# Performance work log

Hardware: AMD Instinct MI355X
Metric: run time of the kernel (lower is better)

Reference implementation:

```python
import jax, jax.numpy as jnp
import numpy as np

B, C = 16384, 2048
DELTA_REL = 0.1


def setup_inputs() -> dict:
    key = jax.random.key(0)
    k1, k2, k3 = jax.random.split(key, 3)
    logits = jax.random.normal(k1, (B, C), dtype=jnp.float32)
    u = jax.random.uniform(k2, (B, C), dtype=jnp.float32)
    lab = (jax.random.uniform(k3, (B, C)) > 0.7).astype(jnp.float32)
    targets = jnp.where(u < 0.4, jnp.float32(jnp.nan), lab)
    return {"logits": logits, "targets": targets, "epoch": 3}


def _large_loss_rejection(logits, targets, epoch):
    unknown = jnp.isnan(targets)
    # unknown_to_negative: NaN -> 0 (negative label)
    t = jnp.where(unknown, 0.0, targets)
    # stable BCE-with-logits: softplus(x) - x*t
    losses = jax.nn.softplus(logits) - logits * t

    # --- no-grad mask construction ---
    ul = jax.lax.stop_gradient(losses) * unknown.astype(losses.dtype)
    percent = jnp.minimum(epoch * DELTA_REL, 1.0).astype(jnp.float32)
    n_unknown = jnp.count_nonzero(ul)
    k = jnp.round(n_unknown.astype(jnp.float32) * percent).astype(jnp.int32)
    k = jnp.maximum(k, 1)
    # k-th largest value of flattened unknown losses = topk(k).values.min()
    sorted_desc = jnp.sort(ul.reshape(-1))[::-1]
    loss_threshold = jax.lax.dynamic_slice(sorted_desc, (k - 1,), (1,))[0]
    lambdas = jnp.where(ul > loss_threshold, 0.0, 1.0)

    return losses * lambdas  # reduction='none'


def reference(logits, targets, epoch):
    return _large_loss_rejection(logits, targets, epoch)
```

## Files before the change

### kernel.cpp

```cpp
#include <hip/hip_runtime.h>
#include <math.h>

typedef float    f32x4 __attribute__((ext_vector_type(4)));
typedef unsigned u32x4 __attribute__((ext_vector_type(4)));

#define HC_OFF     0u
#define H12_OFF    16384u
#define H64_OFF    20480u
#define CTRL_OFF   20544u
#define ZERO_WORDS 20560u
#define CAND_OFF   20560u
#define CAND_CAP   900000u
#define LBUF       2048u

#define FLOOR_BITS 0x36000000u

__device__ __forceinline__ float softplus_exact(float x) {
    float ax = fabsf(x);
    float e = (float)exp(-(double)ax);
    float l = (float)log1p((double)e);
    return fmaxf(x, 0.0f) + l;
}
__device__ __forceinline__ unsigned exact_bits(float x) {
    return __float_as_uint(softplus_exact(x));
}

__device__ __forceinline__ unsigned refine_core(float x, float ax, float e,
                                                float sp) {
    unsigned cb = __float_as_uint(sp);
    float mf = 64.0f + 8.0f * ax;
    if (x < 0.0f) mf += __builtin_amdgcn_rcpf(e);
    bool need = (cb < FLOOR_BITS) || (mf >= 524288.0f);
    if (!need) {
        unsigned m = (unsigned)mf;
        unsigned low = cb & 0xFFFFFu;
        need = (low < m) || (low >= 0x100000u - m);
    }
    if (need) cb = exact_bits(x);
    return cb;
}
__device__ __forceinline__ unsigned refine_A(float x, float* spo) {
    float ax = fabsf(x);
    float e = __expf(-ax);
    float sp = fmaxf(x, 0.0f) + __logf(1.0f + e);
    *spo = sp;
    return refine_core(x, ax, e, sp);
}

__device__ __forceinline__ unsigned kA_elem(float x, float t,
                                            unsigned* __restrict__ sh) {
    float ax = fabsf(x);
    float e = __expf(-ax);
    float sp = fmaxf(x, 0.0f) + __logf(1.0f + e);
    unsigned outb;
    if (isnan(t)) {
        unsigned cb = refine_core(x, ax, e, sp);
        if (cb != 0u) atomicAdd(&sh[cb >> 20], 1u);
        outb = cb;
    } else {
        float loss = sp - x * t;
        outb = __float_as_uint(loss) ^ 0x80000000u;
    }
    return outb;
}

__global__ __launch_bounds__(256) void kA_store_hist(
    const float* __restrict__ lg, const float* __restrict__ tg,
    float* __restrict__ out, unsigned* __restrict__ ws, long long n) {
    __shared__ unsigned sh[4096];
    for (int i = threadIdx.x; i < 4096; i += 256) sh[i] = 0;
    __syncthreads();

    long long n8 = n >> 3;
    long long tid = (long long)blockIdx.x * 256 + threadIdx.x;
    long long stride = (long long)gridDim.x * 256;
    const f32x4* lg4 = (const f32x4*)lg;
    const f32x4* tg4 = (const f32x4*)tg;
    f32x4* out4 = (f32x4*)out;

    long long i = tid;
    f32x4 xa, xb, ta, tb;
    if (i < n8) {
        xa = lg4[2 * i];
        xb = lg4[2 * i + 1];
        ta = __builtin_nontemporal_load(&tg4[2 * i]);
        tb = __builtin_nontemporal_load(&tg4[2 * i + 1]);
    }
    while (i < n8) {
        long long j = i + stride;
        f32x4 nxa, nxb, nta, ntb;
        if (j < n8) {
            nxa = lg4[2 * j];
            nxb = lg4[2 * j + 1];
            nta = __builtin_nontemporal_load(&tg4[2 * j]);
            ntb = __builtin_nontemporal_load(&tg4[2 * j + 1]);
        }
        f32x4 oa, ob_;
        oa.x = __uint_as_float(kA_elem(xa.x, ta.x, sh));
        oa.y = __uint_as_float(kA_elem(xa.y, ta.y, sh));
        oa.z = __uint_as_float(kA_elem(xa.z, ta.z, sh));
        oa.w = __uint_as_float(kA_elem(xa.w, ta.w, sh));
        ob_.x = __uint_as_float(kA_elem(xb.x, tb.x, sh));
        ob_.y = __uint_as_float(kA_elem(xb.y, tb.y, sh));
        ob_.z = __uint_as_float(kA_elem(xb.z, tb.z, sh));
        ob_.w = __uint_as_float(kA_elem(xb.w, tb.w, sh));
        out4[2 * i] = oa;
        out4[2 * i + 1] = ob_;
        xa = nxa; xb = nxb; ta = nta; tb = ntb;
        i = j;
    }
    if (tid == 0) {
        for (long long q = (n8 << 3); q < n; ++q)
            out[q] = __uint_as_float(kA_elem(lg[q], tg[q], sh));
    }
    __syncthreads();
    unsigned* hist12 = ws + H12_OFF;
    for (int q = threadIdx.x; q < 4096; q += 256)
        if (sh[q]) atomicAdd(&hist12[q], sh[q]);
}

__global__ __launch_bounds__(256) void k2_sel12(
    unsigned* __restrict__ ws, const int* __restrict__ epoch_ptr) {
    const unsigned* hist12 = ws + H12_OFF;
    unsigned* ctrl = ws + CTRL_OFF;
    __shared__ unsigned long long chunk[256];
    int t = threadIdx.x;
    unsigned long long s = 0;
    for (int j = 0; j < 16; ++j) s += hist12[t * 16 + j];
    chunk[t] = s;
    __syncthreads();
    if (t == 0) {
        unsigned long long tot = 0;
        for (int c = 0; c < 256; ++c) tot += chunk[c];
        int epoch = epoch_ptr[0];
        float percent = fminf((float)epoch * 0.1f, 1.0f);
        float nf = (float)tot;
        float kr = rintf(nf * percent);
        long long k = (long long)kr;
        if (k < 1) k = 1;

        long long cum = 0;
        int b = -1;
        long long kprime = 0;
        for (int c = 255; c >= 0; --c) {
            if (cum + (long long)chunk[c] >= k) {
                long long cc = cum;
                for (int j = 15; j >= 0; --j) {
                    unsigned v = hist12[c * 16 + j];
                    if (cc + (long long)v >= k) {
                        b = c * 16 + j;
                        kprime = k - cc;
                        break;
                    }
                    cc += v;
                }
                break;
            }
            cum += chunk[c];
        }
        ctrl[0] = (unsigned)b;
        ctrl[1] = (unsigned)kprime;
        if (b < 0) {
            ctrl[2] = 0u;
            ctrl[4] = 0xFFFFFFFFu;
            ctrl[6] = 0u;
        } else {
            unsigned lo12 = (unsigned)b << 20;
            double vlo = (double)__uint_as_float(lo12);
            double vhi = (double)__uint_as_float(lo12 + 0xFFFFFu);
            double mb = 1e9;
            if (vlo > 1e-30) {
                double xlo = vlo + log1p(-exp(-vlo)) - 0.001;
                double xhi = vhi + log1p(-exp(-vhi)) + 0.001;
                double axmax = fmax(fabs(xlo), fabs(xhi));
                mb = 64.0 + 8.0 * ceil(axmax);
                if (xlo < 0.0) mb += exp(fmin(-xlo, 30.0));
                mb *= 2.0;
            }
            ctrl[6] = (mb >= 8192.0) ? 8192u : (unsigned)mb;
        }
    }
}

__global__ __launch_bounds__(256) void kB_hist64(
    const float* __restrict__ lg, const unsigned* __restrict__ ob,
    unsigned* __restrict__ ws, long long n) {
    unsigned b12 = ws[CTRL_OFF + 0];
    if (b12 == 0xFFFFFFFFu) return;
    unsigned lo12 = b12 << 20;
    unsigned hi12 = lo12 + (1u << 20);
    unsigned m = ws[CTRL_OFF + 6];

    __shared__ unsigned sh[64];
    __shared__ float buf[LBUF];
    __shared__ unsigned lcnt, gbase;
    if (threadIdx.x < 64) sh[threadIdx.x] = 0;
    if (threadIdx.x == 0) lcnt = 0;
    __syncthreads();

    float* cand = (float*)(ws + CAND_OFF);
    unsigned* cnt = ws + CTRL_OFF + 3;

    long long n4 = n >> 2;
    long long tid = (long long)blockIdx.x * 256 + threadIdx.x;
    long long stride = (long long)gridDim.x * 256;
    const u32x4* o4 = (const u32x4*)ob;

    long long i = tid;
    u32x4 u4;
    if (i < n4) u4 = o4[i];
    while (i < n4) {
        long long j = i + stride;
        u32x4 nu4;
        if (j < n4) nu4 = o4[j];
        unsigned us[4] = {u4.x, u4.y, u4.z, u4.w};
#pragma unroll
        for (int c = 0; c < 4; ++c) {
            unsigned u = us[c];
            if (u != 0u && u >= lo12 && u < hi12) {
                float x = lg[i * 4 + c];
                unsigned rB = u;
                unsigned d = u & 16383u;
                if (d < m || d >= 16384u - m)
                    rB = exact_bits(x);
                atomicAdd(&sh[(rB >> 14) & 63u], 1u);
                unsigned li = atomicAdd(&lcnt, 1u);
                if (li < LBUF) buf[li] = x;
            }
        }
        u4 = nu4;
        i = j;
    }
    if (tid == 0) {
        for (long long q = (n4 << 2); q < n; ++q) {
            unsigned u = ob[q];
            if (u != 0u && u >= lo12 && u < hi12) {
                float x = lg[q];
                unsigned rB = u;
                unsigned d = u & 16383u;
                if (d < m || d >= 16384u - m) rB = exact_bits(x);
                atomicAdd(&sh[(rB >> 14) & 63u], 1u);
                unsigned idx = atomicAdd(cnt, 1u);
                if (idx < CAND_CAP) cand[idx] = x;
            }
        }
    }
    __syncthreads();
    if (threadIdx.x < 64 && sh[threadIdx.x])
        atomicAdd(&ws[H64_OFF + threadIdx.x], sh[threadIdx.x]);
    if (threadIdx.x == 0) {
        unsigned add = (lcnt > LBUF) ? (CAND_CAP + 1u) : lcnt;
        gbase = atomicAdd(cnt, add);
    }
    __syncthreads();
    unsigned c2 = lcnt < LBUF ? lcnt : LBUF;
    for (unsigned q = threadIdx.x; q < c2; q += 256) {
        unsigned gi = gbase + q;
        if (gi < CAND_CAP) cand[gi] = buf[q];
    }
}

__global__ void k4_sel64(unsigned* __restrict__ ws) {
    unsigned* ctrl = ws + CTRL_OFF;
    if (ctrl[0] == 0xFFFFFFFFu) return;
    if (threadIdx.x == 0) {
        long long kprime = (long long)ctrl[1];
        long long cum = 0;
        int s = 0;
        long long kpp = 1;
        for (int j = 63; j >= 0; --j) {
            unsigned v = ws[H64_OFF + j];
            if (cum + (long long)v >= kprime) {
                s = j;
                kpp = kprime - cum;
                break;
            }
            cum += v;
        }
        ctrl[4] = (ctrl[0] << 20) + ((unsigned)s << 14);
        ctrl[5] = (unsigned)kpp;
    }
}

__global__ __launch_bounds__(256) void kC_histwin(
    const float* __restrict__ lg, const unsigned* __restrict__ ob,
    unsigned* __restrict__ ws, long long n) {
    unsigned wlo = ws[CTRL_OFF + 4];
    if (wlo == 0xFFFFFFFFu) return;
    unsigned whi = wlo + 16384u;
    unsigned m = ws[CTRL_OFF + 6];
    unsigned b12 = ws[CTRL_OFF + 0];
    unsigned lo12 = b12 << 20;
    unsigned hi12 = lo12 + (1u << 20);
    unsigned glo = (wlo - lo12 > m) ? wlo - m : lo12;
    unsigned ghi = (hi12 - whi > m) ? whi + m : hi12;
    unsigned count = ws[CTRL_OFF + 3];

    long long tid = (long long)blockIdx.x * 256 + threadIdx.x;
    long long stride = (long long)gridDim.x * 256;

    if (count <= CAND_CAP) {
        const float* cand = (const float*)(ws + CAND_OFF);
        for (long long i = tid; i < (long long)count; i += stride) {
            float x = cand[i];
            float spd;
            unsigned u = refine_A(x, &spd);
            if (u >= glo && u < ghi) {
                unsigned eb = exact_bits(x);
                unsigned rB = u;
                unsigned d = u & 16383u;
                if (d < m || d >= 16384u - m) rB = eb;
                if (rB >= wlo && rB < whi) {
                    unsigned off = eb - wlo;
                    if (off < 16384u) atomicAdd(&ws[HC_OFF + off], 1u);
                }
            }
        }
    } else {
        long long n4 = n >> 2;
        const u32x4* o4 = (const u32x4*)ob;
        for (long long i = tid; i < n4; i += stride) {
            u32x4 u4 = o4[i];
            unsigned us[4] = {u4.x, u4.y, u4.z, u4.w};
#pragma unroll
            for (int c = 0; c < 4; ++c) {
                unsigned u = us[c];
                if (u != 0u && u >= glo && u < ghi) {
                    float x = lg[i * 4 + c];
                    unsigned eb = exact_bits(x);
                    unsigned rB = u;
                    unsigned d = u & 16383u;
                    if (d < m || d >= 16384u - m) rB = eb;
                    if (rB >= wlo && rB < whi) {
                        unsigned off = eb - wlo;
                        if (off < 16384u) atomicAdd(&ws[HC_OFF + off], 1u);
                    }
                }
            }
        }
        if (tid == 0) {
            for (long long i = (n4 << 2); i < n; ++i) {
                unsigned u = ob[i];
                if (u != 0u && u >= glo && u < ghi) {
                    unsigned eb = exact_bits(lg[i]);
                    unsigned rB = u;
                    unsigned d = u & 16383u;
                    if (d < m || d >= 16384u - m) rB = eb;
                    if (rB >= wlo && rB < whi) {
                        unsigned off = eb - wlo;
                        if (off < 16384u) atomicAdd(&ws[HC_OFF + off], 1u);
                    }
                }
            }
        }
    }
}

__global__ __launch_bounds__(1024) void k6_selwin(unsigned* __restrict__ ws) {
    unsigned* ctrl = ws + CTRL_OFF;
    if (ctrl[4] == 0xFFFFFFFFu) return;
    __shared__ unsigned long long csum[1024];
    int t = threadIdx.x;
    unsigned long long s = 0;
    for (int j = 0; j < 16; ++j) s += ws[HC_OFF + t * 16 + j];
    csum[t] = s;
    __syncthreads();
    if (t == 0) {
        long long kpp = (long long)ctrl[5];
        long long cum = 0;
        int sel = 0;
        long long rem = kpp;
        for (int c = 1023; c >= 0; --c) {
            if (cum + (long long)csum[c] >= kpp) {
                sel = c;
                rem = kpp - cum;
                break;
            }
            cum += csum[c];
        }
        long long cc = 0;
        int bsel = 0;
        for (int j = 15; j >= 0; --j) {
            unsigned v = ws[HC_OFF + sel * 16 + j];
            if (cc + (long long)v >= rem) {
                bsel = j;
                break;
            }
            cc += v;
        }
        ctrl[2] = ctrl[4] + (unsigned)(sel * 16 + bsel);
    }
}

__device__ __forceinline__ unsigned kD_elem(unsigned u, unsigned thr,
                                            unsigned m,
                                            const float* __restrict__ lg,
                                            long long idx) {
    if (u & 0x80000000u) return u ^ 0x80000000u;
    unsigned udiff = (u > thr) ? u - thr : thr - u;
    if (udiff <= m) {
        unsigned eb = exact_bits(lg[idx]);
        return (eb > thr) ? 0u : eb;
    }
    return (u > thr) ? 0u : u;
}

__global__ __launch_bounds__(256) void kD_final(
    const float* __restrict__ lg, unsigned* __restrict__ ob,
    const unsigned* __restrict__ ws, long long n) {
    unsigned thr = ws[CTRL_OFF + 2];
    unsigned m = ws[CTRL_OFF + 6];

    long long n8 = n >> 3;
    long long tid = (long long)blockIdx.x * 256 + threadIdx.x;
    long long stride = (long long)gridDim.x * 256;
    u32x4* o4 = (u32x4*)ob;

    long long i = tid;
    u32x4 ua, ub;
    if (i < n8) {
        ua = o4[2 * i];
        ub = o4[2 * i + 1];
    }
    while (i < n8) {
        long long j = i + stride;
        u32x4 nua, nub;
        if (j < n8) {
            nua = o4[2 * j];
            nub = o4[2 * j + 1];
        }
        u32x4 va, vb;
        long long base = i * 8;
        va.x = kD_elem(ua.x, thr, m, lg, base + 0);
        va.y = kD_elem(ua.y, thr, m, lg, base + 1);
        va.z = kD_elem(ua.z, thr, m, lg, base + 2);
        va.w = kD_elem(ua.w, thr, m, lg, base + 3);
        vb.x = kD_elem(ub.x, thr, m, lg, base + 4);
        vb.y = kD_elem(ub.y, thr, m, lg, base + 5);
        vb.z = kD_elem(ub.z, thr, m, lg, base + 6);
        vb.w = kD_elem(ub.w, thr, m, lg, base + 7);
        __builtin_nontemporal_store(va, &o4[2 * i]);
        __builtin_nontemporal_store(vb, &o4[2 * i + 1]);
        ua = nua; ub = nub;
        i = j;
    }
    if (tid == 0) {
        for (long long q = (n8 << 3); q < n; ++q)
            ob[q] = kD_elem(ob[q], thr, m, lg, q);
    }
}

extern "C" void kernel_launch(void* const* d_in, const int* in_sizes, int n_in,
                              void* d_out, int out_size, void* d_ws, size_t ws_size,
                              hipStream_t stream) {
    const float* lg = (const float*)d_in[0];
    const float* tg = (const float*)d_in[1];
    const int* epoch = (const int*)d_in[2];
    float* out = (float*)d_out;
    unsigned* ob = (unsigned*)d_out;
    unsigned* ws = (unsigned*)d_ws;
    long long n = (long long)in_sizes[0];

    (void)hipMemsetAsync(d_ws, 0, (size_t)ZERO_WORDS * 4, stream);

    const int blocks = 2048, threads = 256;
    kA_store_hist<<<blocks, threads, 0, stream>>>(lg, tg, out, ws, n);
    k2_sel12<<<1, 256, 0, stream>>>(ws, epoch);
    kB_hist64<<<blocks, threads, 0, stream>>>(lg, ob, ws, n);
    k4_sel64<<<1, 64, 0, stream>>>(ws);
    kC_histwin<<<1024, threads, 0, stream>>>(lg, ob, ws, n);
    k6_selwin<<<1, 1024, 0, stream>>>(ws);
    kD_final<<<blocks, threads, 0, stream>>>(lg, ob, ws, n);
}
```

Measured before the change: 242.0 us.

## Estimate threshold window from sampled histogram to avoid extra full passes

Adds a sampling pre-pass (one 8-element unit per 512 elements) that builds a coarse and then a sub-bin histogram of unknown losses to estimate a narrow value window around the k-th largest. The main pass then zeroes elements above the window, counts them, and records the indices of in-window elements into a compact gray list. A small exact-selection stage over that list finds the threshold and fixes up those entries. This replaces the later full passes over the output and logits. If the window estimate fails, a fallback path recomputes from the inputs. It adds several small launches and shared-memory atomics in the main pass in exchange for skipping the heavy full-array passes.

```diff
diff --git a/kernel.cpp b/kernel.cpp
--- a/kernel.cpp
+++ b/kernel.cpp
@@ -4,16 +4,25 @@
 typedef float    f32x4 __attribute__((ext_vector_type(4)));
 typedef unsigned u32x4 __attribute__((ext_vector_type(4)));
 
-#define HC_OFF     0u
+#define HBIG_OFF   0u
 #define H12_OFF    16384u
 #define H64_OFF    20480u
-#define CTRL_OFF   20544u
-#define ZERO_WORDS 20560u
-#define CAND_OFF   20560u
-#define CAND_CAP   900000u
+#define SH12_OFF   20544u
+#define SHSUB_OFF  24640u
+#define CTRL_OFF   24840u
+#define FINE_OFF   24864u
+#define ZERO_WORDS 25376u
+#define GRAY_OFF   25376u
+#define GRAY_CAP   440000u
+#define EB_OFF     (GRAY_OFF + GRAY_CAP)
+#define CAND_OFF   25376u
+#define CAND_CAP   880000u
 #define LBUF       2048u
+#define DELTA_S    2500LL
+#define VMARGIN    16384u
 
 #define FLOOR_BITS 0x36000000u
+
 
 __device__ __forceinline__ float softplus_exact(float x) {
     float ax = fabsf(x);
@@ -39,37 +48,202 @@
     if (need) cb = exact_bits(x);
     return cb;
 }
-__device__ __forceinline__ unsigned refine_A(float x, float* spo) {
+__device__ __forceinline__ unsigned refine_A(float x) {
     float ax = fabsf(x);
     float e = __expf(-ax);
     float sp = fmaxf(x, 0.0f) + __logf(1.0f + e);
-    *spo = sp;
     return refine_core(x, ax, e, sp);
 }
-
-__device__ __forceinline__ unsigned kA_elem(float x, float t,
-                                            unsigned* __restrict__ sh) {
+__device__ __forceinline__ unsigned known_loss_bits(float x, float t) {
     float ax = fabsf(x);
     float e = __expf(-ax);
     float sp = fmaxf(x, 0.0f) + __logf(1.0f + e);
-    unsigned outb;
+    return __float_as_uint(sp - x * t);
+}
+
+__global__ __launch_bounds__(256) void k0a_shist(
+    const float* __restrict__ lg, const float* __restrict__ tg,
+    unsigned* __restrict__ ws, long long n) {
+    __shared__ unsigned sh[4096];
+    for (int i = threadIdx.x; i < 4096; i += 256) sh[i] = 0;
+    __syncthreads();
+    long long units = n >> 9;
+    long long u = (long long)blockIdx.x * 256 + threadIdx.x;
+    if (u < units) {
+        const f32x4* lg4 = (const f32x4*)lg;
+        const f32x4* tg4 = (const f32x4*)tg;
+        long long b = u * 128;
+        f32x4 xa = lg4[b], xb = lg4[b + 1];
+        f32x4 ta = tg4[b], tb = tg4[b + 1];
+        float xs[8] = {xa.x, xa.y, xa.z, xa.w, xb.x, xb.y, xb.z, xb.w};
+        float ts[8] = {ta.x, ta.y, ta.z, ta.w, tb.x, tb.y, tb.z, tb.w};
+#pragma unroll
+        for (int c = 0; c < 8; ++c)
+            if (isnan(ts[c])) {
+                unsigned cb = refine_A(xs[c]);
+                if (cb) atomicAdd(&sh[cb >> 20], 1u);
+            }
+    }
+    __syncthreads();
+    for (int i = threadIdx.x; i < 4096; i += 256)
+        if (sh[i]) atomicAdd(&ws[SH12_OFF + i], sh[i]);
+}
+
+__global__ __launch_bounds__(256) void k0b_sbin(
+    unsigned* __restrict__ ws, const int* __restrict__ epoch_ptr) {
+    const unsigned* sh12 = ws + SH12_OFF;
+    unsigned* ctrl = ws + CTRL_OFF;
+    __shared__ unsigned long long chunk[256];
+    int t = threadIdx.x;
+    unsigned long long s = 0;
+    for (int j = 0; j < 16; ++j) s += sh12[t * 16 + j];
+    chunk[t] = s;
+    __syncthreads();
+    if (t == 0) {
+        unsigned long long tot = 0;
+        for (int c = 0; c < 256; ++c) tot += chunk[c];
+        if (tot == 0) {
+            ctrl[7] = 1u;
+            ctrl[8] = 0u; ctrl[9] = 0u; ctrl[19] = 0u;
+            ctrl[17] = 0u; ctrl[18] = 0u;
+            return;
+        }
+        int epoch = epoch_ptr[0];
+        float percent = fminf((float)epoch * 0.1f, 1.0f);
+        long long ks = (long long)((double)percent * (double)tot + 0.5);
+        if (ks < 1) ks = 1;
+        if (ks > (long long)tot) ks = (long long)tot;
+        long long cum = 0;
+        int bE = 0;
+        for (int c = 255; c >= 0; --c) {
+            if (cum + (long long)chunk[c] >= ks) {
+                long long cc = cum;
+                for (int j = 15; j >= 0; --j) {
+                    unsigned v = sh12[c * 16 + j];
+                    if (cc + (long long)v >= ks) { bE = c * 16 + j; break; }
+                    cc += v;
+                }
+                break;
+            }
+            cum += chunk[c];
+        }
+        ctrl[13] = (unsigned)bE;
+        ctrl[17] = (bE > 0) ? (unsigned)(bE - 1) : 0u;
+        ctrl[18] = (bE < 4095) ? (unsigned)(bE + 1) : 4095u;
+        ctrl[19] = (unsigned)ks;
+    }
+}
+
+__global__ __launch_bounds__(256) void k0c_ssub(
+    const float* __restrict__ lg, const float* __restrict__ tg,
+    unsigned* __restrict__ ws, long long n) {
+    if (ws[CTRL_OFF + 7] != 0u) return;
+    unsigned lob = ws[CTRL_OFF + 17], hib = ws[CTRL_OFF + 18];
+    unsigned rlo = lob << 20, rhi = (hib + 1u) << 20;
+    __shared__ unsigned sh[192];
+    if (threadIdx.x < 192) sh[threadIdx.x] = 0;
+    __syncthreads();
+    long long units = n >> 9;
+    long long u = (long long)blockIdx.x * 256 + threadIdx.x;
+    if (u < units) {
+        const f32x4* lg4 = (const f32x4*)lg;
+        const f32x4* tg4 = (const f32x4*)tg;
+        long long b = u * 128;
+        f32x4 xa = lg4[b], xb = lg4[b + 1];
+        f32x4 ta = tg4[b], tb = tg4[b + 1];
+        float xs[8] = {xa.x, xa.y, xa.z, xa.w, xb.x, xb.y, xb.z, xb.w};
+        float ts[8] = {ta.x, ta.y, ta.z, ta.w, tb.x, tb.y, tb.z, tb.w};
+#pragma unroll
+        for (int c = 0; c < 8; ++c)
+            if (isnan(ts[c])) {
+                unsigned cb = refine_A(xs[c]);
+                if (cb >= rlo && cb < rhi && (hib < 4095u || cb >= rlo))
+                    atomicAdd(&sh[(cb - rlo) >> 14], 1u);
+            }
+    }
+    __syncthreads();
+    if (threadIdx.x < 192 && sh[threadIdx.x])
+        atomicAdd(&ws[SHSUB_OFF + threadIdx.x], sh[threadIdx.x]);
+}
+
+__global__ __launch_bounds__(256) void k0d_window(unsigned* __restrict__ ws) {
+    unsigned* ctrl = ws + CTRL_OFF;
+    if (ctrl[7] != 0u) return;
+    __shared__ unsigned long long red[256];
+    __shared__ unsigned arr[192];
+    int t = threadIdx.x;
+    unsigned hib = ctrl[18];
+    unsigned long long s = 0;
+    for (int b = t; b < 4096; b += 256)
+        if ((unsigned)b > hib) s += ws[SH12_OFF + b];
+    red[t] = s;
+    if (t < 192) arr[t] = ws[SHSUB_OFF + t];
+    __syncthreads();
+    for (int off = 128; off > 0; off >>= 1) {
+        if (t < off) red[t] += red[t + off];
+        __syncthreads();
+    }
+    if (t == 0) {
+        unsigned lob = ctrl[17];
+        unsigned base = lob << 20;
+        int nsub = (int)(hib - lob + 1u) * 64;
+        long long ks = (long long)ctrl[19];
+        long long lo_t = ks - DELTA_S;
+        long long hi_t = ks + DELTA_S;
+        long long cum = (long long)red[0];
+        unsigned est_hi = base + ((unsigned)nsub << 14);
+        unsigned est_lo = base;
+        bool fh = false, fl = false;
+        for (int j = nsub - 1; j >= 0; --j) {
+            if (!fh && cum + (long long)arr[j] > lo_t) {
+                est_hi = base + ((unsigned)(j + 1) << 14);
+                fh = true;
+            }
+            cum += arr[j];
+            if (!fl && cum >= hi_t) {
+                est_lo = base + ((unsigned)j << 14);
+                fl = true;
+            }
+            if (fh && fl) break;
+        }
+        if (!fh) est_hi = base;
+        ctrl[8] = est_lo;
+        ctrl[9] = est_hi;
+    }
+}
+
+__device__ __forceinline__ unsigned kA_elem(float x, float t, unsigned idx,
+                                            unsigned* __restrict__ shh,
+                                            unsigned* __restrict__ sha,
+                                            unsigned* __restrict__ buf,
+                                            unsigned* __restrict__ lcnt,
+                                            unsigned elo, unsigned ehi) {
+    float ax = fabsf(x);
+    float e = __expf(-ax);
+    float sp = fmaxf(x, 0.0f) + __logf(1.0f + e);
     if (isnan(t)) {
         unsigned cb = refine_core(x, ax, e, sp);
-        if (cb != 0u) atomicAdd(&sh[cb >> 20], 1u);
-        outb = cb;
-    } else {
-        float loss = sp - x * t;
-        outb = __float_as_uint(loss) ^ 0x80000000u;
-    }
-    return outb;
-}
-
-__global__ __launch_bounds__(256) void kA_store_hist(
+        if (cb != 0u) atomicAdd(&shh[cb >> 20], 1u);
+        if (cb >= ehi) { atomicAdd(sha, 1u); return 0u; }
+        if (cb >= elo) {
+            unsigned li = atomicAdd(lcnt, 1u);
+            if (li < LBUF) buf[li] = idx;
+        }
+        return cb;
+    }
+    return __float_as_uint(sp - x * t);
+}
+
+__global__ __launch_bounds__(256) void kA_main(
     const float* __restrict__ lg, const float* __restrict__ tg,
     float* __restrict__ out, unsigned* __restrict__ ws, long long n) {
-    __shared__ unsigned sh[4096];
-    for (int i = threadIdx.x; i < 4096; i += 256) sh[i] = 0;
-    __syncthreads();
+    __shared__ unsigned shh[4096];
+    __shared__ unsigned buf[LBUF];
+    __shared__ unsigned lcnt, sha, gbase;
+    for (int i = threadIdx.x; i < 4096; i += 256) shh[i] = 0;
+    if (threadIdx.x == 0) { lcnt = 0; sha = 0; }
+    __syncthreads();
+    unsigned elo = ws[CTRL_OFF + 8], ehi = ws[CTRL_OFF + 9];
 
     long long n8 = n >> 3;
     long long tid = (long long)blockIdx.x * 256 + threadIdx.x;
@@ -81,8 +255,7 @@
     long long i = tid;
     f32x4 xa, xb, ta, tb;
     if (i < n8) {
-        xa = lg4[2 * i];
-        xb = lg4[2 * i + 1];
+        xa = lg4[2 * i]; xb = lg4[2 * i + 1];
         ta = __builtin_nontemporal_load(&tg4[2 * i]);
         tb = __builtin_nontemporal_load(&tg4[2 * i + 1]);
     }
@@ -90,36 +263,47 @@
         long long j = i + stride;
         f32x4 nxa, nxb, nta, ntb;
         if (j < n8) {
-            nxa = lg4[2 * j];
-            nxb = lg4[2 * j + 1];
+            nxa = lg4[2 * j]; nxb = lg4[2 * j + 1];
             nta = __builtin_nontemporal_load(&tg4[2 * j]);
             ntb = __builtin_nontemporal_load(&tg4[2 * j + 1]);
         }
+        unsigned base = (unsigned)(i * 8);
         f32x4 oa, ob_;
-        oa.x = __uint_as_float(kA_elem(xa.x, ta.x, sh));
-        oa.y = __uint_as_float(kA_elem(xa.y, ta.y, sh));
-        oa.z = __uint_as_float(kA_elem(xa.z, ta.z, sh));
-        oa.w = __uint_as_float(kA_elem(xa.w, ta.w, sh));
-        ob_.x = __uint_as_float(kA_elem(xb.x, tb.x, sh));
-        ob_.y = __uint_as_float(kA_elem(xb.y, tb.y, sh));
-        ob_.z = __uint_as_float(kA_elem(xb.z, tb.z, sh));
-        ob_.w = __uint_as_float(kA_elem(xb.w, tb.w, sh));
+        oa.x = __uint_as_float(kA_elem(xa.x, ta.x, base + 0, shh, &sha, buf, &lcnt, elo, ehi));
+        oa.y = __uint_as_float(kA_elem(xa.y, ta.y, base + 1, shh, &sha, buf, &lcnt, elo, ehi));
+        oa.z = __uint_as_float(kA_elem(xa.z, ta.z, base + 2, shh, &sha, buf, &lcnt, elo, ehi));
+        oa.w = __uint_as_float(kA_elem(xa.w, ta.w, base + 3, shh, &sha, buf, &lcnt, elo, ehi));
+        ob_.x = __uint_as_float(kA_elem(xb.x, tb.x, base + 4, shh, &sha, buf, &lcnt, elo, ehi));
+        ob_.y = __uint_as_float(kA_elem(xb.y, tb.y, base + 5, shh, &sha, buf, &lcnt, elo, ehi));
+        ob_.z = __uint_as_float(kA_elem(xb.z, tb.z, base + 6, shh, &sha, buf, &lcnt, elo, ehi));
+        ob_.w = __uint_as_float(kA_elem(xb.w, tb.w, base + 7, shh, &sha, buf, &lcnt, elo, ehi));
         out4[2 * i] = oa;
         out4[2 * i + 1] = ob_;
         xa = nxa; xb = nxb; ta = nta; tb = ntb;
         i = j;
     }
     if (tid == 0) {
-        for (long long q = (n8 << 3); q < n; ++q)
-            out[q] = __uint_as_float(kA_elem(lg[q], tg[q], sh));
-    }
-    __syncthreads();
-    unsigned* hist12 = ws + H12_OFF;
+        for (long long q = (n >> 3) << 3; q < n; ++q)
+            out[q] = __uint_as_float(
+                kA_elem(lg[q], tg[q], (unsigned)q, shh, &sha, buf, &lcnt, elo, ehi));
+    }
+    __syncthreads();
     for (int q = threadIdx.x; q < 4096; q += 256)
-        if (sh[q]) atomicAdd(&hist12[q], sh[q]);
-}
-
-__global__ __launch_bounds__(256) void k2_sel12(
+        if (shh[q]) atomicAdd(&ws[H12_OFF + q], shh[q]);
+    if (threadIdx.x == 0) {
+        if (sha) atomicAdd(&ws[CTRL_OFF + 11], sha);
+        unsigned add = (lcnt > LBUF) ? (GRAY_CAP + 1u) : lcnt;
+        gbase = atomicAdd(&ws[CTRL_OFF + 10], add);
+    }
+    __syncthreads();
+    unsigned c2 = lcnt < LBUF ? lcnt : LBUF;
+    for (unsigned q = threadIdx.x; q < c2; q += 256) {
+        unsigned gi = gbase + q;
+        if (gi < GRAY_CAP) ws[GRAY_OFF + gi] = buf[q];
+    }
+}
+
+__global__ __launch_bounds__(256) void k2_route(
     unsigned* __restrict__ ws, const int* __restrict__ epoch_ptr) {
     const unsigned* hist12 = ws + H12_OFF;
     unsigned* ctrl = ws + CTRL_OFF;
@@ -138,7 +322,6 @@
         float kr = rintf(nf * percent);
         long long k = (long long)kr;
         if (k < 1) k = 1;
-
         long long cum = 0;
         int b = -1;
         long long kprime = 0;
@@ -148,9 +331,7 @@
                 for (int j = 15; j >= 0; --j) {
                     unsigned v = hist12[c * 16 + j];
                     if (cc + (long long)v >= k) {
-                        b = c * 16 + j;
-                        kprime = k - cc;
-                        break;
+                        b = c * 16 + j; kprime = k - cc; break;
                     }
                     cc += v;
                 }
@@ -164,84 +345,204 @@
             ctrl[2] = 0u;
             ctrl[4] = 0xFFFFFFFFu;
             ctrl[6] = 0u;
-        } else {
-            unsigned lo12 = (unsigned)b << 20;
-            double vlo = (double)__uint_as_float(lo12);
-            double vhi = (double)__uint_as_float(lo12 + 0xFFFFFu);
-            double mb = 1e9;
-            if (vlo > 1e-30) {
-                double xlo = vlo + log1p(-exp(-vlo)) - 0.001;
-                double xhi = vhi + log1p(-exp(-vhi)) + 0.001;
-                double axmax = fmax(fabs(xlo), fabs(xhi));
-                mb = 64.0 + 8.0 * ceil(axmax);
-                if (xlo < 0.0) mb += exp(fmin(-xlo, 30.0));
-                mb *= 2.0;
-            }
-            ctrl[6] = (mb >= 8192.0) ? 8192u : (unsigned)mb;
-        }
-    }
-}
-
-__global__ __launch_bounds__(256) void kB_hist64(
-    const float* __restrict__ lg, const unsigned* __restrict__ ob,
+            ctrl[7] = 2u;
+            return;
+        }
+        unsigned lo12 = (unsigned)b << 20;
+        double vlo = (double)__uint_as_float(lo12);
+        double vhi = (double)__uint_as_float(lo12 + 0xFFFFFu);
+        double mb = 1e9;
+        if (vlo > 1e-30) {
+            double xlo = vlo + log1p(-exp(-vlo)) - 0.001;
+            double xhi = vhi + log1p(-exp(-vhi)) + 0.001;
+            double axmax = fmax(fabs(xlo), fabs(xhi));
+            mb = 64.0 + 8.0 * ceil(axmax);
+            if (xlo < 0.0) mb += exp(fmin(-xlo, 30.0));
+            mb *= 2.0;
+        }
+        ctrl[6] = (mb >= 8192.0) ? 8192u : (unsigned)mb;
+        unsigned f = ctrl[7];
+        unsigned g = ctrl[10], a = ctrl[11];
+        unsigned elo = ctrl[8], ehi = ctrl[9];
+        long long rank = k - (long long)a;
+        if (g > GRAY_CAP || rank < 1 || rank > (long long)g ||
+            ehi < elo + 2u * VMARGIN)
+            f = 1u;
+        else {
+            ctrl[12] = (unsigned)rank;
+            unsigned W = ehi - elo;
+            unsigned sft = 0;
+            while (((unsigned long long)16384u << sft) < (unsigned long long)W)
+                ++sft;
+            ctrl[15] = sft;
+        }
+        ctrl[7] = f;
+    }
+}
+
+__global__ __launch_bounds__(256) void G1_exact(
+    const float* __restrict__ lg, unsigned* __restrict__ ws) {
+    if (ws[CTRL_OFF + 7] != 0u) return;
+    unsigned gcount = ws[CTRL_OFF + 10];
+    unsigned elo = ws[CTRL_OFF + 8], ehi = ws[CTRL_OFF + 9];
+    unsigned sft = ws[CTRL_OFF + 15];
+    long long tid = (long long)blockIdx.x * 256 + threadIdx.x;
+    long long stride = (long long)gridDim.x * 256;
+    for (long long g = tid; g < (long long)gcount; g += stride) {
+        unsigned idx = ws[GRAY_OFF + g];
+        unsigned eb = exact_bits(lg[idx]);
+        ws[EB_OFF + g] = eb;
+        unsigned bin = (eb < elo) ? 0u
+                     : (eb >= ehi) ? 16383u : ((eb - elo) >> sft);
+        if (bin > 16383u) bin = 16383u;
+        atomicAdd(&ws[HBIG_OFF + bin], 1u);
+    }
+}
+
+__global__ __launch_bounds__(1024) void G2a_selbin(unsigned* __restrict__ ws) {
+    unsigned* ctrl = ws + CTRL_OFF;
+    if (ctrl[7] != 0u) return;
+    __shared__ unsigned long long csum[1024];
+    int t = threadIdx.x;
+    unsigned long long s = 0;
+    for (int j = 0; j < 16; ++j) s += ws[HBIG_OFF + t * 16 + j];
+    csum[t] = s;
+    __syncthreads();
+    if (t == 0) {
+        long long rank = (long long)ctrl[12];
+        long long cum = 0;
+        int sel = -1;
+        long long rem = 1;
+        for (int c = 1023; c >= 0; --c) {
+            if (cum + (long long)csum[c] >= rank) {
+                long long cc = cum;
+                for (int j = 15; j >= 0; --j) {
+                    unsigned v = ws[HBIG_OFF + c * 16 + j];
+                    if (cc + (long long)v >= rank) {
+                        sel = c * 16 + j; rem = rank - cc; break;
+                    }
+                    cc += v;
+                }
+                break;
+            }
+            cum += csum[c];
+        }
+        if (sel < 0) { ctrl[7] = 1u; return; }
+        ctrl[14] = (unsigned)sel;
+        ctrl[16] = (unsigned)rem;
+    }
+}
+
+__global__ __launch_bounds__(256) void G2b_fine(unsigned* __restrict__ ws) {
+    if (ws[CTRL_OFF + 7] != 0u) return;
+    unsigned gcount = ws[CTRL_OFF + 10];
+    unsigned elo = ws[CTRL_OFF + 8], ehi = ws[CTRL_OFF + 9];
+    unsigned sft = ws[CTRL_OFF + 15];
+    unsigned bsel = ws[CTRL_OFF + 14];
+    long long tid = (long long)blockIdx.x * 256 + threadIdx.x;
+    long long stride = (long long)gridDim.x * 256;
+    for (long long g = tid; g < (long long)gcount; g += stride) {
+        unsigned eb = ws[EB_OFF + g];
+        if (eb >= elo && eb < ehi) {
+            unsigned off = eb - elo;
+            if ((off >> sft) == bsel)
+                atomicAdd(&ws[FINE_OFF + (off - (bsel << sft))], 1u);
+        }
+    }
+}
+
+__global__ __launch_bounds__(512) void G2c_thr(unsigned* __restrict__ ws) {
+    unsigned* ctrl = ws + CTRL_OFF;
+    if (ctrl[7] != 0u) return;
+    __shared__ unsigned fine[512];
+    int t = threadIdx.x;
+    unsigned sft = ctrl[15];
+    unsigned binw = 1u << sft;
+    if (binw > 512u) { if (t == 0) ctrl[7] = 1u; return; }
+    if ((unsigned)t < binw) fine[t] = ws[FINE_OFF + t];
+    __syncthreads();
+    if (t == 0) {
+        unsigned elo = ctrl[8], ehi = ctrl[9];
+        unsigned binlo = elo + (ctrl[14] << sft);
+        long long rem = (long long)ctrl[16];
+        long long cum = 0;
+        bool found = false;
+        unsigned thr = 0;
+        for (int o = (int)binw - 1; o >= 0; --o) {
+            cum += fine[o];
+            if (cum >= rem) { thr = binlo + (unsigned)o; found = true; break; }
+        }
+        if (!found || thr < elo + VMARGIN || thr > ehi - VMARGIN)
+            ctrl[7] = 1u;
+        else
+            ctrl[2] = thr;
+    }
+}
+
+__global__ __launch_bounds__(256) void kD_fix(
+    unsigned* __restrict__ ob, const unsigned* __restrict__ ws) {
+    if (ws[CTRL_OFF + 7] != 0u) return;
+    unsigned gcount = ws[CTRL_OFF + 10];
+    unsigned thr = ws[CTRL_OFF + 2];
+    long long tid = (long long)blockIdx.x * 256 + threadIdx.x;
+    long long stride = (long long)gridDim.x * 256;
+    for (long long g = tid; g < (long long)gcount; g += stride) {
+        if (ws[EB_OFF + g] > thr) ob[ws[GRAY_OFF + g]] = 0u;
+    }
+}
+
+__global__ __launch_bounds__(256) void fkB(
+    const float* __restrict__ lg, const float* __restrict__ tg,
     unsigned* __restrict__ ws, long long n) {
+    if (ws[CTRL_OFF + 7] != 1u) return;
     unsigned b12 = ws[CTRL_OFF + 0];
     if (b12 == 0xFFFFFFFFu) return;
-    unsigned lo12 = b12 << 20;
-    unsigned hi12 = lo12 + (1u << 20);
+    unsigned lo12 = b12 << 20, hi12 = lo12 + (1u << 20);
     unsigned m = ws[CTRL_OFF + 6];
-
     __shared__ unsigned sh[64];
     __shared__ float buf[LBUF];
     __shared__ unsigned lcnt, gbase;
     if (threadIdx.x < 64) sh[threadIdx.x] = 0;
     if (threadIdx.x == 0) lcnt = 0;
     __syncthreads();
-
     float* cand = (float*)(ws + CAND_OFF);
     unsigned* cnt = ws + CTRL_OFF + 3;
-
     long long n4 = n >> 2;
     long long tid = (long long)blockIdx.x * 256 + threadIdx.x;
     long long stride = (long long)gridDim.x * 256;
-    const u32x4* o4 = (const u32x4*)ob;
-
-    long long i = tid;
-    u32x4 u4;
-    if (i < n4) u4 = o4[i];
-    while (i < n4) {
-        long long j = i + stride;
-        u32x4 nu4;
-        if (j < n4) nu4 = o4[j];
-        unsigned us[4] = {u4.x, u4.y, u4.z, u4.w};
+    const f32x4* lg4 = (const f32x4*)lg;
+    const f32x4* tg4 = (const f32x4*)tg;
+    for (long long i = tid; i < n4; i += stride) {
+        f32x4 x4 = lg4[i], t4 = tg4[i];
+        float xs[4] = {x4.x, x4.y, x4.z, x4.w};
+        float ts[4] = {t4.x, t4.y, t4.z, t4.w};
 #pragma unroll
         for (int c = 0; c < 4; ++c) {
-            unsigned u = us[c];
-            if (u != 0u && u >= lo12 && u < hi12) {
-                float x = lg[i * 4 + c];
-                unsigned rB = u;
-                unsigned d = u & 16383u;
-                if (d < m || d >= 16384u - m)
-                    rB = exact_bits(x);
-                atomicAdd(&sh[(rB >> 14) & 63u], 1u);
-                unsigned li = atomicAdd(&lcnt, 1u);
-                if (li < LBUF) buf[li] = x;
-            }
-        }
-        u4 = nu4;
-        i = j;
+            if (isnan(ts[c])) {
+                float x = xs[c];
+                unsigned cb = refine_A(x);
+                if (cb >= lo12 && cb < hi12) {
+                    unsigned d = cb & 16383u;
+                    unsigned rB = (d < m || d >= 16384u - m) ? exact_bits(x) : cb;
+                    atomicAdd(&sh[(rB >> 14) & 63u], 1u);
+                    unsigned li = atomicAdd(&lcnt, 1u);
+                    if (li < LBUF) buf[li] = x;
+                }
+            }
+        }
     }
     if (tid == 0) {
         for (long long q = (n4 << 2); q < n; ++q) {
-            unsigned u = ob[q];
-            if (u != 0u && u >= lo12 && u < hi12) {
+            if (isnan(tg[q])) {
                 float x = lg[q];
-                unsigned rB = u;
-                unsigned d = u & 16383u;
-                if (d < m || d >= 16384u - m) rB = exact_bits(x);
-                atomicAdd(&sh[(rB >> 14) & 63u], 1u);
-                unsigned idx = atomicAdd(cnt, 1u);
-                if (idx < CAND_CAP) cand[idx] = x;
+                unsigned cb = refine_A(x);
+                if (cb >= lo12 && cb < hi12) {
+                    unsigned d = cb & 16383u;
+                    unsigned rB = (d < m || d >= 16384u - m) ? exact_bits(x) : cb;
+                    atomicAdd(&sh[(rB >> 14) & 63u], 1u);
+                    unsigned idx = atomicAdd(cnt, 1u);
+                    if (idx < CAND_CAP) cand[idx] = x;
+                }
             }
         }
     }
@@ -260,8 +561,9 @@
     }
 }
 
-__global__ void k4_sel64(unsigned* __restrict__ ws) {
+__global__ void fk4(unsigned* __restrict__ ws) {
     unsigned* ctrl = ws + CTRL_OFF;
+    if (ctrl[7] != 1u) return;
     if (ctrl[0] == 0xFFFFFFFFu) return;
     if (threadIdx.x == 0) {
         long long kprime = (long long)ctrl[1];
@@ -270,11 +572,7 @@
         long long kpp = 1;
         for (int j = 63; j >= 0; --j) {
             unsigned v = ws[H64_OFF + j];
-            if (cum + (long long)v >= kprime) {
-                s = j;
-                kpp = kprime - cum;
-                break;
-            }
+            if (cum + (long long)v >= kprime) { s = j; kpp = kprime - cum; break; }
             cum += v;
         }
         ctrl[4] = (ctrl[0] << 20) + ((unsigned)s << 14);
@@ -282,87 +580,63 @@
     }
 }
 
-__global__ __launch_bounds__(256) void kC_histwin(
-    const float* __restrict__ lg, const unsigned* __restrict__ ob,
+__global__ __launch_bounds__(256) void fkC(
+    const float* __restrict__ lg, const float* __restrict__ tg,
     unsigned* __restrict__ ws, long long n) {
+    if (ws[CTRL_OFF + 7] != 1u) return;
     unsigned wlo = ws[CTRL_OFF + 4];
     if (wlo == 0xFFFFFFFFu) return;
     unsigned whi = wlo + 16384u;
     unsigned m = ws[CTRL_OFF + 6];
     unsigned b12 = ws[CTRL_OFF + 0];
-    unsigned lo12 = b12 << 20;
-    unsigned hi12 = lo12 + (1u << 20);
+    unsigned lo12 = b12 << 20, hi12 = lo12 + (1u << 20);
     unsigned glo = (wlo - lo12 > m) ? wlo - m : lo12;
     unsigned ghi = (hi12 - whi > m) ? whi + m : hi12;
     unsigned count = ws[CTRL_OFF + 3];
-
     long long tid = (long long)blockIdx.x * 256 + threadIdx.x;
     long long stride = (long long)gridDim.x * 256;
-
     if (count <= CAND_CAP) {
         const float* cand = (const float*)(ws + CAND_OFF);
         for (long long i = tid; i < (long long)count; i += stride) {
             float x = cand[i];
-            float spd;
-            unsigned u = refine_A(x, &spd);
+            unsigned u = refine_A(x);
             if (u >= glo && u < ghi) {
                 unsigned eb = exact_bits(x);
-                unsigned rB = u;
                 unsigned d = u & 16383u;
-                if (d < m || d >= 16384u - m) rB = eb;
+                unsigned rB = (d < m || d >= 16384u - m) ? eb : u;
                 if (rB >= wlo && rB < whi) {
                     unsigned off = eb - wlo;
-                    if (off < 16384u) atomicAdd(&ws[HC_OFF + off], 1u);
+                    if (off < 16384u) atomicAdd(&ws[HBIG_OFF + off], 1u);
                 }
             }
         }
     } else {
-        long long n4 = n >> 2;
-        const u32x4* o4 = (const u32x4*)ob;
-        for (long long i = tid; i < n4; i += stride) {
-            u32x4 u4 = o4[i];
-            unsigned us[4] = {u4.x, u4.y, u4.z, u4.w};
-#pragma unroll
-            for (int c = 0; c < 4; ++c) {
-                unsigned u = us[c];
-                if (u != 0u && u >= glo && u < ghi) {
-                    float x = lg[i * 4 + c];
+        for (long long q = tid; q < n; q += stride) {
+            if (isnan(tg[q])) {
+                float x = lg[q];
+                unsigned u = refine_A(x);
+                if (u >= glo && u < ghi) {
                     unsigned eb = exact_bits(x);
-                    unsigned rB = u;
                     unsigned d = u & 16383u;
-                    if (d < m || d >= 16384u - m) rB = eb;
+                    unsigned rB = (d < m || d >= 16384u - m) ? eb : u;
                     if (rB >= wlo && rB < whi) {
                         unsigned off = eb - wlo;
-                        if (off < 16384u) atomicAdd(&ws[HC_OFF + off], 1u);
+                        if (off < 16384u) atomicAdd(&ws[HBIG_OFF + off], 1u);
                     }
                 }
             }
         }
-        if (tid == 0) {
-            for (long long i = (n4 << 2); i < n; ++i) {
-                unsigned u = ob[i];
-                if (u != 0u && u >= glo && u < ghi) {
-                    unsigned eb = exact_bits(lg[i]);
-                    unsigned rB = u;
-                    unsigned d = u & 16383u;
-                    if (d < m || d >= 16384u - m) rB = eb;
-                    if (rB >= wlo && rB < whi) {
-                        unsigned off = eb - wlo;
-                        if (off < 16384u) atomicAdd(&ws[HC_OFF + off], 1u);
-                    }
-                }
-            }
-        }
-    }
-}
-
-__global__ __launch_bounds__(1024) void k6_selwin(unsigned* __restrict__ ws) {
+    }
+}
+
+__global__ __launch_bounds__(1024) void fk6(unsigned* __restrict__ ws) {
     unsigned* ctrl = ws + CTRL_OFF;
+    if (ctrl[7] != 1u) return;
     if (ctrl[4] == 0xFFFFFFFFu) return;
     __shared__ unsigned long long csum[1024];
     int t = threadIdx.x;
     unsigned long long s = 0;
-    for (int j = 0; j < 16; ++j) s += ws[HC_OFF + t * 16 + j];
+    for (int j = 0; j < 16; ++j) s += ws[HBIG_OFF + t * 16 + j];
     csum[t] = s;
     __syncthreads();
     if (t == 0) {
@@ -371,82 +645,73 @@
         int sel = 0;
         long long rem = kpp;
         for (int c = 1023; c >= 0; --c) {
-            if (cum + (long long)csum[c] >= kpp) {
-                sel = c;
-                rem = kpp - cum;
-                break;
-            }
+            if (cum + (long long)csum[c] >= kpp) { sel = c; rem = kpp - cum; break; }
             cum += csum[c];
         }
         long long cc = 0;
         int bsel = 0;
         for (int j = 15; j >= 0; --j) {
-            unsigned v = ws[HC_OFF + sel * 16 + j];
-            if (cc + (long long)v >= rem) {
-                bsel = j;
-                break;
-            }
+            unsigned v = ws[HBIG_OFF + sel * 16 + j];
+            if (cc + (long long)v >= rem) { bsel = j; break; }
             cc += v;
         }
         ctrl[2] = ctrl[4] + (unsigned)(sel * 16 + bsel);
     }
 }
 
-__device__ __forceinline__ unsigned kD_elem(unsigned u, unsigned thr,
-                                            unsigned m,
-                                            const float* __restrict__ lg,
-                                            long long idx) {
-    if (u & 0x80000000u) return u ^ 0x80000000u;
-    unsigned udiff = (u > thr) ? u - thr : thr - u;
-    if (udiff <= m) {
-        unsigned eb = exact_bits(lg[idx]);
-        return (eb > thr) ? 0u : eb;
-    }
-    return (u > thr) ? 0u : u;
-}
-
-__global__ __launch_bounds__(256) void kD_final(
-    const float* __restrict__ lg, unsigned* __restrict__ ob,
-    const unsigned* __restrict__ ws, long long n) {
+__global__ __launch_bounds__(256) void fkD(
+    const float* __restrict__ lg, const float* __restrict__ tg,
+    float* __restrict__ out, const unsigned* __restrict__ ws, long long n) {
+    if (ws[CTRL_OFF + 7] != 1u) return;
     unsigned thr = ws[CTRL_OFF + 2];
     unsigned m = ws[CTRL_OFF + 6];
-
-    long long n8 = n >> 3;
+    long long n4 = n >> 2;
     long long tid = (long long)blockIdx.x * 256 + threadIdx.x;
     long long stride = (long long)gridDim.x * 256;
-    u32x4* o4 = (u32x4*)ob;
-
-    long long i = tid;
-    u32x4 ua, ub;
-    if (i < n8) {
-        ua = o4[2 * i];
-        ub = o4[2 * i + 1];
-    }
-    while (i < n8) {
-        long long j = i + stride;
-        u32x4 nua, nub;
-        if (j < n8) {
-            nua = o4[2 * j];
-            nub = o4[2 * j + 1];
-        }
-        u32x4 va, vb;
-        long long base = i * 8;
-        va.x = kD_elem(ua.x, thr, m, lg, base + 0);
-        va.y = kD_elem(ua.y, thr, m, lg, base + 1);
-        va.z = kD_elem(ua.z, thr, m, lg, base + 2);
-        va.w = kD_elem(ua.w, thr, m, lg, base + 3);
-        vb.x = kD_elem(ub.x, thr, m, lg, base + 4);
-        vb.y = kD_elem(ub.y, thr, m, lg, base + 5);
-        vb.z = kD_elem(ub.z, thr, m, lg, base + 6);
-        vb.w = kD_elem(ub.w, thr, m, lg, base + 7);
-        __builtin_nontemporal_store(va, &o4[2 * i]);
-        __builtin_nontemporal_store(vb, &o4[2 * i + 1]);
-        ua = nua; ub = nub;
-        i = j;
+    const f32x4* lg4 = (const f32x4*)lg;
+    const f32x4* tg4 = (const f32x4*)tg;
+    f32x4* out4 = (f32x4*)out;
+    for (long long i = tid; i < n4; i += stride) {
+        f32x4 x4 = lg4[i], t4 = tg4[i];
+        float xs[4] = {x4.x, x4.y, x4.z, x4.w};
+        float ts[4] = {t4.x, t4.y, t4.z, t4.w};
+        f32x4 o;
+        float os[4];
+#pragma unroll
+        for (int c = 0; c < 4; ++c) {
+            float x = xs[c], t = ts[c];
+            if (isnan(t)) {
+                unsigned cb = refine_A(x);
+                unsigned udiff = (cb > thr) ? cb - thr : thr - cb;
+                unsigned r;
+                if (udiff <= m) {
+                    unsigned eb = exact_bits(x);
+                    r = (eb > thr) ? 0u : eb;
+                } else {
+                    r = (cb > thr) ? 0u : cb;
+                }
+                os[c] = __uint_as_float(r);
+            } else {
+                os[c] = __uint_as_float(known_loss_bits(x, t));
+            }
+        }
+        o.x = os[0]; o.y = os[1]; o.z = os[2]; o.w = os[3];
+        out4[i] = o;
     }
     if (tid == 0) {
-        for (long long q = (n8 << 3); q < n; ++q)
-            ob[q] = kD_elem(ob[q], thr, m, lg, q);
+        for (long long q = (n4 << 2); q < n; ++q) {
+            float x = lg[q], t = tg[q];
+            if (isnan(t)) {
+                unsigned cb = refine_A(x);
+                unsigned udiff = (cb > thr) ? cb - thr : thr - cb;
+                unsigned eb, r;
+                if (udiff <= m) { eb = exact_bits(x); r = (eb > thr) ? 0u : eb; }
+                else r = (cb > thr) ? 0u : cb;
+                out[q] = __uint_as_float(r);
+            } else {
+                out[q] = __uint_as_float(known_loss_bits(x, t));
+            }
+        }
     }
 }
 
@@ -463,12 +728,20 @@
 
     (void)hipMemsetAsync(d_ws, 0, (size_t)ZERO_WORDS * 4, stream);
 
-    const int blocks = 2048, threads = 256;
-    kA_store_hist<<<blocks, threads, 0, stream>>>(lg, tg, out, ws, n);
-    k2_sel12<<<1, 256, 0, stream>>>(ws, epoch);
-    kB_hist64<<<blocks, threads, 0, stream>>>(lg, ob, ws, n);
-    k4_sel64<<<1, 64, 0, stream>>>(ws);
-    kC_histwin<<<1024, threads, 0, stream>>>(lg, ob, ws, n);
-    k6_selwin<<<1, 1024, 0, stream>>>(ws);
-    kD_final<<<blocks, threads, 0, stream>>>(lg, ob, ws, n);
-}
+    k0a_shist<<<256, 256, 0, stream>>>(lg, tg, ws, n);
+    k0b_sbin<<<1, 256, 0, stream>>>(ws, epoch);
+    k0c_ssub<<<256, 256, 0, stream>>>(lg, tg, ws, n);
+    k0d_window<<<1, 256, 0, stream>>>(ws);
+    kA_main<<<2048, 256, 0, stream>>>(lg, tg, out, ws, n);
+    k2_route<<<1, 256, 0, stream>>>(ws, epoch);
+    G1_exact<<<128, 256, 0, stream>>>(lg, ws);
+    G2a_selbin<<<1, 1024, 0, stream>>>(ws);
+    G2b_fine<<<128, 256, 0, stream>>>(ws);
+    G2c_thr<<<1, 512, 0, stream>>>(ws);
+    kD_fix<<<128, 256, 0, stream>>>(ob, ws);
+    fkB<<<2048, 256, 0, stream>>>(lg, tg, ws, n);
+    fk4<<<1, 64, 0, stream>>>(ws);
+    fkC<<<1024, 256, 0, stream>>>(lg, tg, ws, n);
+    fk6<<<1, 1024, 0, stream>>>(ws);
+    fkD<<<2048, 256, 0, stream>>>(lg, tg, out, ws, n);
+}
```

New measurement: 266.7 us. 1.1x slower.
